# Kernel optimization log

Hardware: AMD Instinct MI355X
Metric: run time of the kernel (lower is better)

The kernel has to match this reference:

```python
import jax, jax.numpy as jnp
import numpy as np

B, L, D, H = 4, 2048, 1024, 16
DH = D // H
SCALE = 1.0 / float(np.sqrt(DH))


def setup_inputs() -> dict:
    key = jax.random.key(0)
    ks = jax.random.split(key, 11)
    s = 0.02
    return {
        "q": jax.random.normal(ks[0], (B, L, D), jnp.float32),
        "k": jax.random.normal(ks[1], (B, L, D), jnp.float32),
        "v": jax.random.normal(ks[2], (B, L, D), jnp.float32),
        "Wq": jax.random.normal(ks[3], (D, D), jnp.float32) * s,
        "bq": jnp.zeros((D,), jnp.float32),
        "Wk": jax.random.normal(ks[4], (D, D), jnp.float32) * s,
        "bk": jnp.zeros((D,), jnp.float32),
        "Wv": jax.random.normal(ks[5], (D, D), jnp.float32) * s,
        "bv": jnp.zeros((D,), jnp.float32),
        "Wo": jax.random.normal(ks[6], (D, D), jnp.float32) * s,
        "bo": jnp.zeros((D,), jnp.float32),
    }


def _split_heads(x):
    # (B, L, D) -> (B, H, L, DH)
    b, l, _ = x.shape
    return x.reshape(b, l, H, DH).transpose(0, 2, 1, 3)


def reference(q, k, v, Wq, bq, Wk, bk, Wv, bv, Wo, bo):
    # torch Linear: y = x @ W.T + b
    qh = _split_heads(q @ Wq.T + bq)
    kh = _split_heads(k @ Wk.T + bk)
    vh = _split_heads(v @ Wv.T + bv)
    # Blocked loop in original == full attention: every q block sees all K/V.
    scores = jnp.einsum("bhqd,bhkd->bhqk", qh, kh) * SCALE
    attn = jax.nn.softmax(scores, axis=-1)  # dropout=0 (eval) -> identity
    out = jnp.einsum("bhqk,bhkd->bhqd", attn, vh)
    out = out.transpose(0, 2, 1, 3).reshape(q.shape[0], q.shape[1], D)
    return out @ Wo.T + bo
```

## Files before the change

kernel.cpp:

```cpp
#include <hip/hip_runtime.h>
#include <hip/hip_bf16.h>
#include <stdint.h>

#define NB  4
#define SEQ 2048
#define DIM 1024
#define NH  16
#define DHD 64
#define LOG2E 1.44269504088896340736f

typedef short short8 __attribute__((ext_vector_type(8)));
typedef float f32x4  __attribute__((ext_vector_type(4)));

__device__ __forceinline__ unsigned short f2bf(float f) {
  union { float f; uint32_t u; } x; x.f = f;
  uint32_t u = x.u;
  uint32_t r = (u + 0x7fffu + ((u >> 16) & 1u)) >> 16;
  return (unsigned short)r;
}

__device__ __forceinline__ uint32_t cvt_pk_bf16(float lo, float hi) {
  uint32_t r;
  asm("v_cvt_pk_bf16_f32 %0, %1, %2" : "=v"(r) : "v"(lo), "v"(hi));
  return r;
}

__device__ __forceinline__ void gload16(const void* g, void* l) {
  __builtin_amdgcn_global_load_lds(
      (const __attribute__((address_space(1))) uint32_t*)g,
      (__attribute__((address_space(3))) uint32_t*)l, 16, 0, 0);
}

__global__ void cvt_f32_bf16(const float* __restrict__ in,
                             unsigned short* __restrict__ out, int n4) {
  int i = blockIdx.x * blockDim.x + threadIdx.x;
  int stride = gridDim.x * blockDim.x;
  for (int j = i; j < n4; j += stride) {
    float4 v = reinterpret_cast<const float4*>(in)[j];
    ushort4 o;
    o.x = f2bf(v.x); o.y = f2bf(v.y); o.z = f2bf(v.z); o.w = f2bf(v.w);
    reinterpret_cast<ushort4*>(out)[j] = o;
  }
}

template <int MODE>
__global__ __launch_bounds__(256, 2) void gemm_bt(
    const unsigned short* __restrict__ A,
    const unsigned short* __restrict__ Bm,
    const float* __restrict__ bias,
    float* __restrict__ Cf,
    unsigned short* __restrict__ Cb,
    int M, int N, int K, float scale) {
  __shared__ uint4 smem[4096];

  const int tid  = threadIdx.x;
  const int lane = tid & 63;
  const int wid  = tid >> 6;
  const int cpx  = gridDim.x >> 3;
  const int wg   = (blockIdx.x & 7) * cpx + (blockIdx.x >> 3);
  const int nbn  = N >> 7;
  const int bm   = wg / nbn;
  const int bn   = wg % nbn;
  const int wrow = (wid >> 1) * 64;
  const int wcol = (wid & 1) * 64;

  f32x4 acc[4][4] = {};

  const unsigned short* pa[4];
  const unsigned short* pb[4];
  uint4* la[4];
  uint4* lb[4];
#pragma unroll
  for (int i = 0; i < 4; ++i) {
    int c   = tid + (i << 8);
    int row = c >> 3;
    int kc  = (c & 7) ^ (row & 7);
    pa[i] = A  + (size_t)(bm * 128 + row) * K + kc * 8;
    pb[i] = Bm + (size_t)(bn * 128 + row) * K + kc * 8;
    la[i] = smem + c;
    lb[i] = smem + 2048 + c;
  }
  auto stage = [&](int kt, int buf) {
#pragma unroll
    for (int i = 0; i < 4; ++i) {
      gload16(pa[i] + kt * 64, la[i] + buf * 1024);
      gload16(pb[i] + kt * 64, lb[i] + buf * 1024);
    }
  };

  stage(0, 0);
  __syncthreads();

  const int NT = K >> 6;
  for (int kt = 0; kt < NT; ++kt) {
    const int cur = kt & 1;
    if (kt + 1 < NT) stage(kt + 1, cur ^ 1);

#pragma unroll
    for (int s = 0; s < 2; ++s) {
      short8 af[4], bfr[4];
#pragma unroll
      for (int mt = 0; mt < 4; ++mt) {
        int row = wrow + mt * 16 + (lane & 15);
        int ch  = ((s << 2) + (lane >> 4)) ^ (row & 7);
        af[mt]  = __builtin_bit_cast(short8, smem[cur * 1024 + row * 8 + ch]);
      }
#pragma unroll
      for (int nt = 0; nt < 4; ++nt) {
        int row = wcol + nt * 16 + (lane & 15);
        int ch  = ((s << 2) + (lane >> 4)) ^ (row & 7);
        bfr[nt] = __builtin_bit_cast(short8, smem[2048 + cur * 1024 + row * 8 + ch]);
      }
      __builtin_amdgcn_s_setprio(1);
#pragma unroll
      for (int mt = 0; mt < 4; ++mt)
#pragma unroll
        for (int nt = 0; nt < 4; ++nt)
          acc[mt][nt] = __builtin_amdgcn_mfma_f32_16x16x32_bf16(af[mt], bfr[nt], acc[mt][nt], 0, 0, 0);
      __builtin_amdgcn_s_setprio(0);
    }
    __syncthreads();
  }

  if (MODE == 0) {
    float* cf = (float*)smem;
#pragma unroll
    for (int nt = 0; nt < 4; ++nt) {
      int tcol = wcol + nt * 16 + (lane & 15);
      float bv = bias[bn * 128 + tcol];
#pragma unroll
      for (int mt = 0; mt < 4; ++mt)
#pragma unroll
        for (int r = 0; r < 4; ++r) {
          int trow = wrow + mt * 16 + (lane >> 4) * 4 + r;
          cf[trow * 128 + tcol] = acc[mt][nt][r] + bv;
        }
    }
    __syncthreads();
#pragma unroll
    for (int it = 0; it < 16; ++it) {
      int idx = tid + it * 256;
      int row = idx >> 5, seg = idx & 31;
      uint4 val = ((uint4*)cf)[idx];
      *reinterpret_cast<uint4*>(Cf + (size_t)(bm * 128 + row) * N + bn * 128 + seg * 4) = val;
    }
  } else if (MODE == 1) {
    unsigned short* cb = (unsigned short*)smem;
#pragma unroll
    for (int nt = 0; nt < 4; ++nt) {
      int tcol = wcol + nt * 16 + (lane & 15);
      float bv = bias[bn * 128 + tcol];
#pragma unroll
      for (int mt = 0; mt < 4; ++mt)
#pragma unroll
        for (int r = 0; r < 4; ++r) {
          int trow = wrow + mt * 16 + (lane >> 4) * 4 + r;
          cb[trow * 128 + tcol] = f2bf((acc[mt][nt][r] + bv) * scale);
        }
    }
    __syncthreads();
#pragma unroll
    for (int it = 0; it < 8; ++it) {
      int idx = tid + it * 256;
      int row = idx >> 4, seg = idx & 15;
      uint4 val = ((uint4*)cb)[idx];
      int gcol = bn * 128 + seg * 8;
      int h = gcol >> 6, dh = gcol & 63;
      int grow = bm * 128 + row;
      int b = grow >> 11, lq = grow & 2047;
      *reinterpret_cast<uint4*>(Cb + ((size_t)((b << 4) + h) * SEQ + lq) * DHD + dh) = val;
    }
  } else {
    unsigned short* cb = (unsigned short*)smem;
#pragma unroll
    for (int nt = 0; nt < 4; ++nt) {
      int tcol = wcol + nt * 16 + (lane & 15);
      float bv = bias[bn * 128 + tcol];
#pragma unroll
      for (int mt = 0; mt < 4; ++mt) {
        int trow0 = wrow + mt * 16 + (lane >> 4) * 4;
        uint2 pk;
        pk.x = cvt_pk_bf16((acc[mt][nt][0] + bv) * scale, (acc[mt][nt][1] + bv) * scale);
        pk.y = cvt_pk_bf16((acc[mt][nt][2] + bv) * scale, (acc[mt][nt][3] + bv) * scale);
        *reinterpret_cast<uint2*>(cb + tcol * 128 + trow0) = pk;
      }
    }
    __syncthreads();
#pragma unroll
    for (int it = 0; it < 8; ++it) {
      int idx = tid + it * 256;
      int col = idx >> 4, seg = idx & 15;
      uint4 val = ((uint4*)cb)[idx];
      int gcol = bn * 128 + col;
      int h = gcol >> 6, dh = gcol & 63;
      int grow = bm * 128 + seg * 8;
      int b = grow >> 11, lq = grow & 2047;
      *reinterpret_cast<uint4*>(Cb + ((size_t)((b << 4) + h) * DHD + dh) * SEQ + lq) = val;
    }
  }
}

__global__ __launch_bounds__(256, 3) void attn_kernel(
    const unsigned short* __restrict__ Qh,
    const unsigned short* __restrict__ Kh,
    const unsigned short* __restrict__ Vt,
    unsigned short* __restrict__ O) {
  __shared__ uint4 Kls[2][512];
  __shared__ uint4 Vls[2][512];
  __shared__ uint4 Pls[4][32 * 9];

  const int tid  = threadIdx.x;
  const int lane = tid & 63;
  const int wid  = tid >> 6;
  const int wg   = (blockIdx.x & 7) * 128 + (blockIdx.x >> 3);
  const int bh   = wg >> 4;
  const int qt   = wg & 15;
  const int qloc = lane & 15;
  const int grp  = lane >> 4;
  const int q7   = qloc & 7;

  const unsigned short* Qb = Qh + (size_t)bh * SEQ * DHD;
  const unsigned short* Kb = Kh + (size_t)bh * SEQ * DHD;
  const unsigned short* Vb = Vt + (size_t)bh * DHD * SEQ;

  const unsigned short* pk[2];
  const unsigned short* pv[2];
  uint4* lk[2];
  uint4* lv[2];
#pragma unroll
  for (int i = 0; i < 2; ++i) {
    int c   = tid + (i << 8);
    int row = c >> 3;
    int kc  = (c & 7) ^ (row & 7);
    pk[i] = Kb + (size_t)row * DHD + kc * 8;
    pv[i] = Vb + (size_t)row * SEQ + kc * 8;
    lk[i] = &Kls[0][c];
    lv[i] = &Vls[0][c];
  }
  auto stage = [&](int kt, int buf) {
#pragma unroll
    for (int i = 0; i < 2; ++i) {
      gload16(pk[i] + (size_t)kt * 64 * DHD, lk[i] + buf * 512);
      gload16(pv[i] + kt * 64,               lv[i] + buf * 512);
    }
  };

  stage(0, 0);

  short8 qf[2][2];
#pragma unroll
  for (int qb = 0; qb < 2; ++qb) {
    int qrow = qt * 128 + wid * 32 + qb * 16 + qloc;
#pragma unroll
    for (int s = 0; s < 2; ++s)
      qf[qb][s] = *reinterpret_cast<const short8*>(Qb + (size_t)qrow * DHD + s * 32 + grp * 8);
  }

  const short8 ones = {0x3F80, 0x3F80, 0x3F80, 0x3F80, 0x3F80, 0x3F80, 0x3F80, 0x3F80};
  char* pwb = (char*)&Pls[wid][0];

  __syncthreads();

  float logbias = 0.f;
  f32x4 lsum[2] = {};
  f32x4 acc_o[4][2] = {};

  const int NT = SEQ / 64;
  for (int kt = 0; kt < NT; ++kt) {
    const int cur = kt & 1;
    if (kt + 1 < NT) stage(kt + 1, cur ^ 1);

    f32x4 sc[4][2];
    __builtin_amdgcn_s_setprio(1);
#pragma unroll
    for (int j = 0; j < 4; ++j) {
      short8 kf[2];
#pragma unroll
      for (int s = 0; s < 2; ++s) {
        int krow = j * 16 + qloc;
        int ch   = ((s << 2) + grp) ^ q7;
        kf[s] = __builtin_bit_cast(short8, Kls[cur][krow * 8 + ch]);
      }
#pragma unroll
      for (int qb = 0; qb < 2; ++qb) {
        f32x4 a = {0.f, 0.f, 0.f, 0.f};
        a = __builtin_amdgcn_mfma_f32_16x16x32_bf16(kf[0], qf[qb][0], a, 0, 0, 0);
        a = __builtin_amdgcn_mfma_f32_16x16x32_bf16(kf[1], qf[qb][1], a, 0, 0, 0);
        sc[j][qb] = a;
      }
    }
    __builtin_amdgcn_s_setprio(0);

#pragma unroll
    for (int j = 0; j < 4; ++j)
#pragma unroll
      for (int qb = 0; qb < 2; ++qb) {
        float p0 = exp2f(sc[j][qb][0] + logbias);
        float p1 = exp2f(sc[j][qb][1] + logbias);
        float p2 = exp2f(sc[j][qb][2] + logbias);
        float p3 = exp2f(sc[j][qb][3] + logbias);
        uint2 w;
        w.x = cvt_pk_bf16(p0, p1);
        w.y = cvt_pk_bf16(p2, p3);
        *(uint2*)(pwb + (qb * 16 + qloc) * 144 + j * 32 + grp * 8) = w;
      }

    short8 pf[2][2];
#pragma unroll
    for (int qb = 0; qb < 2; ++qb)
#pragma unroll
      for (int t = 0; t < 2; ++t)
        pf[qb][t] = *(const short8*)(pwb + (qb * 16 + qloc) * 144 + t * 64 + grp * 16);

    __builtin_amdgcn_s_setprio(1);
#pragma unroll
    for (int db = 0; db < 4; ++db) {
      short8 vf[2];
#pragma unroll
      for (int t = 0; t < 2; ++t) {
        int vrow = db * 16 + qloc;
        int ch   = ((t << 2) + grp) ^ q7;
        vf[t] = __builtin_bit_cast(short8, Vls[cur][vrow * 8 + ch]);
      }
#pragma unroll
      for (int qb = 0; qb < 2; ++qb) {
        acc_o[db][qb] = __builtin_amdgcn_mfma_f32_16x16x32_bf16(vf[0], pf[qb][0], acc_o[db][qb], 0, 0, 0);
        acc_o[db][qb] = __builtin_amdgcn_mfma_f32_16x16x32_bf16(vf[1], pf[qb][1], acc_o[db][qb], 0, 0, 0);
      }
    }
#pragma unroll
    for (int qb = 0; qb < 2; ++qb) {
      lsum[qb] = __builtin_amdgcn_mfma_f32_16x16x32_bf16(ones, pf[qb][0], lsum[qb], 0, 0, 0);
      lsum[qb] = __builtin_amdgcn_mfma_f32_16x16x32_bf16(ones, pf[qb][1], lsum[qb], 0, 0, 0);
    }
    __builtin_amdgcn_s_setprio(0);

    if (__any(fmaxf(lsum[0][0], lsum[1][0]) > 7.9e28f)) {
      const float ds = 5.421010862e-20f;
      logbias -= 64.f;
#pragma unroll
      for (int db = 0; db < 4; ++db)
#pragma unroll
        for (int qb = 0; qb < 2; ++qb)
#pragma unroll
          for (int r = 0; r < 4; ++r) acc_o[db][qb][r] *= ds;
#pragma unroll
      for (int qb = 0; qb < 2; ++qb)
#pragma unroll
        for (int r = 0; r < 4; ++r) lsum[qb][r] *= ds;
    }

    __syncthreads();
  }

  const float inv0 = 1.0f / lsum[0][0];
  const float inv1 = 1.0f / lsum[1][0];
#pragma unroll
  for (int db = 0; db < 4; ++db)
#pragma unroll
    for (int qb = 0; qb < 2; ++qb) {
      float inv = qb ? inv1 : inv0;
      uint2 w;
      w.x = cvt_pk_bf16(acc_o[db][qb][0] * inv, acc_o[db][qb][1] * inv);
      w.y = cvt_pk_bf16(acc_o[db][qb][2] * inv, acc_o[db][qb][3] * inv);
      *(uint2*)(pwb + (qb * 16 + qloc) * 144 + db * 32 + grp * 8) = w;
    }
  const int b = bh >> 4, h = bh & 15;
#pragma unroll
  for (int pass = 0; pass < 4; ++pass) {
    int idx = pass * 64 + lane;
    int row = idx >> 3;
    int ck  = idx & 7;
    uint4 val = *(const uint4*)(pwb + row * 144 + ck * 16);
    int rowg = qt * 128 + wid * 32 + row;
    *reinterpret_cast<uint4*>(O + ((size_t)(b * SEQ + rowg)) * DIM + (h << 6) + ck * 8) = val;
  }
}

extern "C" void kernel_launch(void* const* d_in, const int* in_sizes, int n_in,
                              void* d_out, int out_size, void* d_ws, size_t ws_size,
                              hipStream_t stream) {
  (void)in_sizes; (void)n_in; (void)out_size; (void)ws_size;
  const float* q  = (const float*)d_in[0];
  const float* k  = (const float*)d_in[1];
  const float* v  = (const float*)d_in[2];
  const float* Wq = (const float*)d_in[3];
  const float* bq = (const float*)d_in[4];
  const float* Wk = (const float*)d_in[5];
  const float* bk = (const float*)d_in[6];
  const float* Wv = (const float*)d_in[7];
  const float* bv = (const float*)d_in[8];
  const float* Wo = (const float*)d_in[9];
  const float* bo = (const float*)d_in[10];
  float* out = (float*)d_out;

  char* ws = (char*)d_ws;
  const size_t MB = 1024 * 1024;
  unsigned short* X   = (unsigned short*)(ws + 0);
  unsigned short* WX  = (unsigned short*)(ws + 16 * MB);
  unsigned short* Qhp = (unsigned short*)(ws + 18 * MB);
  unsigned short* Khp = (unsigned short*)(ws + 34 * MB);
  unsigned short* Vtp = (unsigned short*)(ws + 50 * MB);

  const int nTok = NB * SEQ * DIM;
  const int nW   = DIM * DIM;
  const int M    = NB * SEQ;
  dim3 gg((M / 128) * (DIM / 128));

  cvt_f32_bf16<<<2048, 256, 0, stream>>>(q, X, nTok / 4);
  cvt_f32_bf16<<<1024, 256, 0, stream>>>(Wq, WX, nW / 4);
  gemm_bt<1><<<gg, 256, 0, stream>>>(X, WX, bq, nullptr, Qhp, M, DIM, DIM, 0.125f * LOG2E);
  cvt_f32_bf16<<<2048, 256, 0, stream>>>(k, X, nTok / 4);
  cvt_f32_bf16<<<1024, 256, 0, stream>>>(Wk, WX, nW / 4);
  gemm_bt<1><<<gg, 256, 0, stream>>>(X, WX, bk, nullptr, Khp, M, DIM, DIM, 1.0f);
  cvt_f32_bf16<<<2048, 256, 0, stream>>>(v, X, nTok / 4);
  cvt_f32_bf16<<<1024, 256, 0, stream>>>(Wv, WX, nW / 4);
  gemm_bt<2><<<gg, 256, 0, stream>>>(X, WX, bv, nullptr, Vtp, M, DIM, DIM, 1.0f);
  attn_kernel<<<NB * NH * (SEQ / 128), 256, 0, stream>>>(Qhp, Khp, Vtp, X);
  cvt_f32_bf16<<<1024, 256, 0, stream>>>(Wo, WX, nW / 4);
  gemm_bt<0><<<gg, 256, 0, stream>>>(X, WX, bo, out, nullptr, M, DIM, DIM, 1.0f);
}
```

Baseline: 246.1 us.

## Double attention workgroup to 512 threads sharing K/V tiles across 256 queries

The attention kernel now launches 512-thread workgroups covering 256 query rows, so each staged K/V tile in shared memory is reused by eight waves instead of four. Each thread now issues one global-to-LDS load per tile instead of two. The logbias add is folded into the MFMA accumulator initialisation, which removes a separate add before each exp2. In exchange there are half as many workgroups, and block-wide barriers must synchronise more waves.

```diff
diff --git a/kernel.cpp b/kernel.cpp
--- a/kernel.cpp
+++ b/kernel.cpp
@@ -200,21 +200,21 @@
   }
 }
 
-__global__ __launch_bounds__(256, 3) void attn_kernel(
+__global__ __launch_bounds__(512, 4) void attn_kernel(
     const unsigned short* __restrict__ Qh,
     const unsigned short* __restrict__ Kh,
     const unsigned short* __restrict__ Vt,
     unsigned short* __restrict__ O) {
   __shared__ uint4 Kls[2][512];
   __shared__ uint4 Vls[2][512];
-  __shared__ uint4 Pls[4][32 * 9];
+  __shared__ uint4 Pls[8][32 * 9];
 
   const int tid  = threadIdx.x;
   const int lane = tid & 63;
   const int wid  = tid >> 6;
-  const int wg   = (blockIdx.x & 7) * 128 + (blockIdx.x >> 3);
-  const int bh   = wg >> 4;
-  const int qt   = wg & 15;
+  const int wg   = (blockIdx.x & 7) * 64 + (blockIdx.x >> 3);
+  const int bh   = wg >> 3;
+  const int qt   = wg & 7;
   const int qloc = lane & 15;
   const int grp  = lane >> 4;
   const int q7   = qloc & 7;
@@ -223,26 +223,13 @@
   const unsigned short* Kb = Kh + (size_t)bh * SEQ * DHD;
   const unsigned short* Vb = Vt + (size_t)bh * DHD * SEQ;
 
-  const unsigned short* pk[2];
-  const unsigned short* pv[2];
-  uint4* lk[2];
-  uint4* lv[2];
-#pragma unroll
-  for (int i = 0; i < 2; ++i) {
-    int c   = tid + (i << 8);
-    int row = c >> 3;
-    int kc  = (c & 7) ^ (row & 7);
-    pk[i] = Kb + (size_t)row * DHD + kc * 8;
-    pv[i] = Vb + (size_t)row * SEQ + kc * 8;
-    lk[i] = &Kls[0][c];
-    lv[i] = &Vls[0][c];
-  }
+  const int srow = tid >> 3;
+  const int skc  = (tid & 7) ^ (srow & 7);
+  const unsigned short* pk0 = Kb + (size_t)srow * DHD + skc * 8;
+  const unsigned short* pv0 = Vb + (size_t)srow * SEQ + skc * 8;
   auto stage = [&](int kt, int buf) {
-#pragma unroll
-    for (int i = 0; i < 2; ++i) {
-      gload16(pk[i] + (size_t)kt * 64 * DHD, lk[i] + buf * 512);
-      gload16(pv[i] + kt * 64,               lv[i] + buf * 512);
-    }
+    gload16(pk0 + (size_t)kt * 64 * DHD, &Kls[buf][tid]);
+    gload16(pv0 + kt * 64,               &Vls[buf][tid]);
   };
 
   stage(0, 0);
@@ -250,7 +237,7 @@
   short8 qf[2][2];
 #pragma unroll
   for (int qb = 0; qb < 2; ++qb) {
-    int qrow = qt * 128 + wid * 32 + qb * 16 + qloc;
+    int qrow = qt * 256 + wid * 32 + qb * 16 + qloc;
 #pragma unroll
     for (int s = 0; s < 2; ++s)
       qf[qb][s] = *reinterpret_cast<const short8*>(Qb + (size_t)qrow * DHD + s * 32 + grp * 8);
@@ -283,7 +270,7 @@
       }
 #pragma unroll
       for (int qb = 0; qb < 2; ++qb) {
-        f32x4 a = {0.f, 0.f, 0.f, 0.f};
+        f32x4 a = {logbias, logbias, logbias, logbias};
         a = __builtin_amdgcn_mfma_f32_16x16x32_bf16(kf[0], qf[qb][0], a, 0, 0, 0);
         a = __builtin_amdgcn_mfma_f32_16x16x32_bf16(kf[1], qf[qb][1], a, 0, 0, 0);
         sc[j][qb] = a;
@@ -295,10 +282,10 @@
     for (int j = 0; j < 4; ++j)
 #pragma unroll
       for (int qb = 0; qb < 2; ++qb) {
-        float p0 = exp2f(sc[j][qb][0] + logbias);
-        float p1 = exp2f(sc[j][qb][1] + logbias);
-        float p2 = exp2f(sc[j][qb][2] + logbias);
-        float p3 = exp2f(sc[j][qb][3] + logbias);
+        float p0 = exp2f(sc[j][qb][0]);
+        float p1 = exp2f(sc[j][qb][1]);
+        float p2 = exp2f(sc[j][qb][2]);
+        float p3 = exp2f(sc[j][qb][3]);
         uint2 w;
         w.x = cvt_pk_bf16(p0, p1);
         w.y = cvt_pk_bf16(p2, p3);
@@ -372,7 +359,7 @@
     int row = idx >> 3;
     int ck  = idx & 7;
     uint4 val = *(const uint4*)(pwb + row * 144 + ck * 16);
-    int rowg = qt * 128 + wid * 32 + row;
+    int rowg = qt * 256 + wid * 32 + row;
     *reinterpret_cast<uint4*>(O + ((size_t)(b * SEQ + rowg)) * DIM + (h << 6) + ck * 8) = val;
   }
 }
@@ -416,7 +403,7 @@
   cvt_f32_bf16<<<2048, 256, 0, stream>>>(v, X, nTok / 4);
   cvt_f32_bf16<<<1024, 256, 0, stream>>>(Wv, WX, nW / 4);
   gemm_bt<2><<<gg, 256, 0, stream>>>(X, WX, bv, nullptr, Vtp, M, DIM, DIM, 1.0f);
-  attn_kernel<<<NB * NH * (SEQ / 128), 256, 0, stream>>>(Qhp, Khp, Vtp, X);
+  attn_kernel<<<NB * NH * (SEQ / 256), 512, 0, stream>>>(Qhp, Khp, Vtp, X);
   cvt_f32_bf16<<<1024, 256, 0, stream>>>(Wo, WX, nW / 4);
   gemm_bt<0><<<gg, 256, 0, stream>>>(X, WX, bo, out, nullptr, M, DIM, DIM, 1.0f);
 }
```

Measured after the change: 233.5 us. -5.1%, faster.

## Double attention query tile per workgroup to 256 rows, reusing K/V fragments

Applied to the files above, without the earlier changes.

Each attention workgroup now handles 256 query rows (64 per wave) instead of 128, so every K/V tile staged in LDS and loaded into registers serves four query sub-blocks instead of two. K and V fragments are loaded once per tile and reused across all query sub-blocks. The logbias is folded into the MFMA accumulator initialisation, which removes one add per score. The cost is higher register pressure (launch bounds lowered to 2 blocks per CU), a larger P buffer in LDS, and half as many workgroups (512), which cuts parallelism and occupancy.

```diff
diff --git a/kernel.cpp b/kernel.cpp
--- a/kernel.cpp
+++ b/kernel.cpp
@@ -200,21 +200,21 @@
   }
 }
 
-__global__ __launch_bounds__(256, 3) void attn_kernel(
+__global__ __launch_bounds__(256, 2) void attn_kernel(
     const unsigned short* __restrict__ Qh,
     const unsigned short* __restrict__ Kh,
     const unsigned short* __restrict__ Vt,
     unsigned short* __restrict__ O) {
   __shared__ uint4 Kls[2][512];
   __shared__ uint4 Vls[2][512];
-  __shared__ uint4 Pls[4][32 * 9];
+  __shared__ uint4 Pls[4][64 * 9];
 
   const int tid  = threadIdx.x;
   const int lane = tid & 63;
   const int wid  = tid >> 6;
-  const int wg   = (blockIdx.x & 7) * 128 + (blockIdx.x >> 3);
-  const int bh   = wg >> 4;
-  const int qt   = wg & 15;
+  const int wg   = (blockIdx.x & 7) * 64 + (blockIdx.x >> 3);
+  const int bh   = wg >> 3;
+  const int qt   = wg & 7;
   const int qloc = lane & 15;
   const int grp  = lane >> 4;
   const int q7   = qloc & 7;
@@ -247,10 +247,10 @@
 
   stage(0, 0);
 
-  short8 qf[2][2];
-#pragma unroll
-  for (int qb = 0; qb < 2; ++qb) {
-    int qrow = qt * 128 + wid * 32 + qb * 16 + qloc;
+  short8 qf[4][2];
+#pragma unroll
+  for (int qb = 0; qb < 4; ++qb) {
+    int qrow = qt * 256 + wid * 64 + qb * 16 + qloc;
 #pragma unroll
     for (int s = 0; s < 2; ++s)
       qf[qb][s] = *reinterpret_cast<const short8*>(Qb + (size_t)qrow * DHD + s * 32 + grp * 8);
@@ -262,90 +262,82 @@
   __syncthreads();
 
   float logbias = 0.f;
-  f32x4 lsum[2] = {};
-  f32x4 acc_o[4][2] = {};
+  f32x4 lsum[4] = {};
+  f32x4 acc_o[4][4] = {};
 
   const int NT = SEQ / 64;
   for (int kt = 0; kt < NT; ++kt) {
     const int cur = kt & 1;
     if (kt + 1 < NT) stage(kt + 1, cur ^ 1);
 
-    f32x4 sc[4][2];
-    __builtin_amdgcn_s_setprio(1);
-#pragma unroll
-    for (int j = 0; j < 4; ++j) {
-      short8 kf[2];
+    short8 kf[4][2];
+#pragma unroll
+    for (int j = 0; j < 4; ++j)
 #pragma unroll
       for (int s = 0; s < 2; ++s) {
         int krow = j * 16 + qloc;
         int ch   = ((s << 2) + grp) ^ q7;
-        kf[s] = __builtin_bit_cast(short8, Kls[cur][krow * 8 + ch]);
-      }
-#pragma unroll
-      for (int qb = 0; qb < 2; ++qb) {
-        f32x4 a = {0.f, 0.f, 0.f, 0.f};
-        a = __builtin_amdgcn_mfma_f32_16x16x32_bf16(kf[0], qf[qb][0], a, 0, 0, 0);
-        a = __builtin_amdgcn_mfma_f32_16x16x32_bf16(kf[1], qf[qb][1], a, 0, 0, 0);
-        sc[j][qb] = a;
-      }
-    }
-    __builtin_amdgcn_s_setprio(0);
-
-#pragma unroll
-    for (int j = 0; j < 4; ++j)
-#pragma unroll
-      for (int qb = 0; qb < 2; ++qb) {
-        float p0 = exp2f(sc[j][qb][0] + logbias);
-        float p1 = exp2f(sc[j][qb][1] + logbias);
-        float p2 = exp2f(sc[j][qb][2] + logbias);
-        float p3 = exp2f(sc[j][qb][3] + logbias);
+        kf[j][s] = __builtin_bit_cast(short8, Kls[cur][krow * 8 + ch]);
+      }
+
+#pragma unroll
+    for (int qb = 0; qb < 4; ++qb) {
+      f32x4 sc[4];
+      __builtin_amdgcn_s_setprio(1);
+#pragma unroll
+      for (int j = 0; j < 4; ++j) {
+        f32x4 a = {logbias, logbias, logbias, logbias};
+        a = __builtin_amdgcn_mfma_f32_16x16x32_bf16(kf[j][0], qf[qb][0], a, 0, 0, 0);
+        a = __builtin_amdgcn_mfma_f32_16x16x32_bf16(kf[j][1], qf[qb][1], a, 0, 0, 0);
+        sc[j] = a;
+      }
+      __builtin_amdgcn_s_setprio(0);
+#pragma unroll
+      for (int j = 0; j < 4; ++j) {
         uint2 w;
-        w.x = cvt_pk_bf16(p0, p1);
-        w.y = cvt_pk_bf16(p2, p3);
+        w.x = cvt_pk_bf16(exp2f(sc[j][0]), exp2f(sc[j][1]));
+        w.y = cvt_pk_bf16(exp2f(sc[j][2]), exp2f(sc[j][3]));
         *(uint2*)(pwb + (qb * 16 + qloc) * 144 + j * 32 + grp * 8) = w;
       }
-
-    short8 pf[2][2];
-#pragma unroll
-    for (int qb = 0; qb < 2; ++qb)
-#pragma unroll
-      for (int t = 0; t < 2; ++t)
-        pf[qb][t] = *(const short8*)(pwb + (qb * 16 + qloc) * 144 + t * 64 + grp * 16);
-
-    __builtin_amdgcn_s_setprio(1);
-#pragma unroll
-    for (int db = 0; db < 4; ++db) {
-      short8 vf[2];
+    }
+
+    short8 vf[4][2];
+#pragma unroll
+    for (int db = 0; db < 4; ++db)
 #pragma unroll
       for (int t = 0; t < 2; ++t) {
         int vrow = db * 16 + qloc;
         int ch   = ((t << 2) + grp) ^ q7;
-        vf[t] = __builtin_bit_cast(short8, Vls[cur][vrow * 8 + ch]);
-      }
-#pragma unroll
-      for (int qb = 0; qb < 2; ++qb) {
-        acc_o[db][qb] = __builtin_amdgcn_mfma_f32_16x16x32_bf16(vf[0], pf[qb][0], acc_o[db][qb], 0, 0, 0);
-        acc_o[db][qb] = __builtin_amdgcn_mfma_f32_16x16x32_bf16(vf[1], pf[qb][1], acc_o[db][qb], 0, 0, 0);
-      }
-    }
-#pragma unroll
-    for (int qb = 0; qb < 2; ++qb) {
-      lsum[qb] = __builtin_amdgcn_mfma_f32_16x16x32_bf16(ones, pf[qb][0], lsum[qb], 0, 0, 0);
-      lsum[qb] = __builtin_amdgcn_mfma_f32_16x16x32_bf16(ones, pf[qb][1], lsum[qb], 0, 0, 0);
-    }
-    __builtin_amdgcn_s_setprio(0);
-
-    if (__any(fmaxf(lsum[0][0], lsum[1][0]) > 7.9e28f)) {
+        vf[db][t] = __builtin_bit_cast(short8, Vls[cur][vrow * 8 + ch]);
+      }
+
+#pragma unroll
+    for (int qb = 0; qb < 4; ++qb) {
+      short8 pf0 = *(const short8*)(pwb + (qb * 16 + qloc) * 144 + 0 * 64 + grp * 16);
+      short8 pf1 = *(const short8*)(pwb + (qb * 16 + qloc) * 144 + 1 * 64 + grp * 16);
+      __builtin_amdgcn_s_setprio(1);
+#pragma unroll
+      for (int db = 0; db < 4; ++db) {
+        acc_o[db][qb] = __builtin_amdgcn_mfma_f32_16x16x32_bf16(vf[db][0], pf0, acc_o[db][qb], 0, 0, 0);
+        acc_o[db][qb] = __builtin_amdgcn_mfma_f32_16x16x32_bf16(vf[db][1], pf1, acc_o[db][qb], 0, 0, 0);
+      }
+      lsum[qb] = __builtin_amdgcn_mfma_f32_16x16x32_bf16(ones, pf0, lsum[qb], 0, 0, 0);
+      lsum[qb] = __builtin_amdgcn_mfma_f32_16x16x32_bf16(ones, pf1, lsum[qb], 0, 0, 0);
+      __builtin_amdgcn_s_setprio(0);
+    }
+
+    float lm = fmaxf(fmaxf(lsum[0][0], lsum[1][0]), fmaxf(lsum[2][0], lsum[3][0]));
+    if (__any(lm > 7.9e28f)) {
       const float ds = 5.421010862e-20f;
       logbias -= 64.f;
 #pragma unroll
       for (int db = 0; db < 4; ++db)
 #pragma unroll
-        for (int qb = 0; qb < 2; ++qb)
+        for (int qb = 0; qb < 4; ++qb)
 #pragma unroll
           for (int r = 0; r < 4; ++r) acc_o[db][qb][r] *= ds;
 #pragma unroll
-      for (int qb = 0; qb < 2; ++qb)
+      for (int qb = 0; qb < 4; ++qb)
 #pragma unroll
         for (int r = 0; r < 4; ++r) lsum[qb][r] *= ds;
     }
@@ -353,26 +345,26 @@
     __syncthreads();
   }
 
-  const float inv0 = 1.0f / lsum[0][0];
-  const float inv1 = 1.0f / lsum[1][0];
+  float inv[4];
+#pragma unroll
+  for (int qb = 0; qb < 4; ++qb) inv[qb] = 1.0f / lsum[qb][0];
 #pragma unroll
   for (int db = 0; db < 4; ++db)
 #pragma unroll
-    for (int qb = 0; qb < 2; ++qb) {
-      float inv = qb ? inv1 : inv0;
+    for (int qb = 0; qb < 4; ++qb) {
       uint2 w;
-      w.x = cvt_pk_bf16(acc_o[db][qb][0] * inv, acc_o[db][qb][1] * inv);
-      w.y = cvt_pk_bf16(acc_o[db][qb][2] * inv, acc_o[db][qb][3] * inv);
+      w.x = cvt_pk_bf16(acc_o[db][qb][0] * inv[qb], acc_o[db][qb][1] * inv[qb]);
+      w.y = cvt_pk_bf16(acc_o[db][qb][2] * inv[qb], acc_o[db][qb][3] * inv[qb]);
       *(uint2*)(pwb + (qb * 16 + qloc) * 144 + db * 32 + grp * 8) = w;
     }
   const int b = bh >> 4, h = bh & 15;
 #pragma unroll
-  for (int pass = 0; pass < 4; ++pass) {
+  for (int pass = 0; pass < 8; ++pass) {
     int idx = pass * 64 + lane;
     int row = idx >> 3;
     int ck  = idx & 7;
     uint4 val = *(const uint4*)(pwb + row * 144 + ck * 16);
-    int rowg = qt * 128 + wid * 32 + row;
+    int rowg = qt * 256 + wid * 64 + row;
     *reinterpret_cast<uint4*>(O + ((size_t)(b * SEQ + rowg)) * DIM + (h << 6) + ck * 8) = val;
   }
 }
@@ -416,7 +408,7 @@
   cvt_f32_bf16<<<2048, 256, 0, stream>>>(v, X, nTok / 4);
   cvt_f32_bf16<<<1024, 256, 0, stream>>>(Wv, WX, nW / 4);
   gemm_bt<2><<<gg, 256, 0, stream>>>(X, WX, bv, nullptr, Vtp, M, DIM, DIM, 1.0f);
-  attn_kernel<<<NB * NH * (SEQ / 128), 256, 0, stream>>>(Qhp, Khp, Vtp, X);
+  attn_kernel<<<NB * NH * (SEQ / 256), 256, 0, stream>>>(Qhp, Khp, Vtp, X);
   cvt_f32_bf16<<<1024, 256, 0, stream>>>(Wo, WX, nW / 4);
   gemm_bt<0><<<gg, 256, 0, stream>>>(X, WX, bo, out, nullptr, M, DIM, DIM, 1.0f);
 }
```

Measured after the change: 237.4 us. -3.5%, faster.
